# Optimization experiments

Hardware: AMD Instinct MI355X
Metric: run time of the kernel (lower is better)

The kernel has to match this reference:

```python
import jax, jax.numpy as jnp
import numpy as np

B, S, HID = 2, 2048, 2048
H, K, D = 32, 8, 64          # query heads, kv heads, head_dim
G = H // K                   # GQA group size
ROPE_MSCALE = 1.2            # constant rope_mscale applied to q and k
SM_SCALE = 1.0 / (D ** 0.5)  # flash_attn default softmax scale


def rotate_half(x):
    h = x.shape[-1] // 2
    return jnp.concatenate([-x[..., h:], x[..., :h]], axis=-1)


def setup_inputs() -> dict:
    key = jax.random.key(0)
    k1, k2, k3, k4 = jax.random.split(key, 4)
    hidden_states = jax.random.normal(k1, (B, S, HID), dtype=jnp.float32)
    # standard rotary tables: cos/sin of shape [S, D]
    inv_freq = 1.0 / (10000.0 ** (jnp.arange(0, D, 2, dtype=jnp.float32) / D))
    freqs = jnp.outer(jnp.arange(S, dtype=jnp.float32), inv_freq)  # [S, D/2]
    emb = jnp.concatenate([freqs, freqs], axis=-1)                 # [S, D]
    cos, sin = jnp.cos(emb), jnp.sin(emb)
    per_head_scale = 1.0 + 0.1 * jax.random.normal(k2, (B, H), dtype=jnp.float32)
    Wqkv = jax.random.normal(k3, ((H + 2 * K) * D, HID), dtype=jnp.float32) * (HID ** -0.5)
    Wo = jax.random.normal(k4, (HID, H * D), dtype=jnp.float32) * ((H * D) ** -0.5)
    return {"cos": cos, "sin": sin, "hidden_states": hidden_states,
            "per_head_scale": per_head_scale, "Wqkv": Wqkv, "Wo": Wo}


def reference(cos, sin, hidden_states, per_head_scale, Wqkv, Wo):
    # fused QKV projection (CastedLinear, no bias)
    qkv = jnp.einsum('bsh,oh->bso', hidden_states, Wqkv)          # [B,S,(H+2K)*D]
    qkv = qkv.reshape(B, S, H + 2 * K, D)
    q = qkv[:, :, :H]                 # [B,S,H,D]
    k = qkv[:, :, H:H + K]            # [B,S,K,D]
    v = qkv[:, :, H + K:]             # [B,S,K,D]
    # rotary embedding: cos/sin [S,D] -> broadcast over heads via [S,1,D]
    c = cos[:, None, :]
    s_ = sin[:, None, :]
    q = q * c + rotate_half(q) * s_
    k = k * c + rotate_half(k) * s_
    # rope_mscale
    q = q * ROPE_MSCALE
    k = k * ROPE_MSCALE
    # per-head scale on queries: [B,H] -> [B,1,H,1]
    q = q * per_head_scale[:, None, :, None]
    # GQA attention without materializing repeated K/V: group query heads
    qg = q.reshape(B, S, K, G, D)
    scores = jnp.einsum('bqkgd,bskd->bkgqs', qg, k) * SM_SCALE    # [B,K,G,Sq,Sk]
    causal = jnp.arange(S)[:, None] >= jnp.arange(S)[None, :]     # [Sq,Sk]
    scores = jnp.where(causal, scores, jnp.finfo(scores.dtype).min)
    probs = jax.nn.softmax(scores, axis=-1)
    out = jnp.einsum('bkgqs,bskd->bqkgd', probs, v).reshape(B, S, H * D)
    return jnp.einsum('bso,ho->bsh', out, Wo)                     # o_proj
```

## Files before the change

### kernel.cpp

```cpp
#include <hip/hip_runtime.h>
#include <stdint.h>

typedef unsigned short u16;
typedef short short8 __attribute__((ext_vector_type(8)));
typedef float f32x4 __attribute__((ext_vector_type(4)));
typedef uint32_t u32x4 __attribute__((ext_vector_type(4)));

#define S_LEN 2048
#define NQH 32
#define NKH 8
#define DHD 64

__device__ __forceinline__ float b2f(u16 u){
  union { uint32_t i; float f; } c; c.i = ((uint32_t)u) << 16; return c.f;
}
__device__ __forceinline__ u16 f2b(float f){
  union { float f; uint32_t i; } c; c.f = f;
  uint32_t r = c.i + 0x7fffu + ((c.i >> 16) & 1u);
  return (u16)(r >> 16);
}
__device__ __forceinline__ uint32_t cvt_pk_bf16(float lo, float hi){
  uint32_t r;
  asm("v_cvt_pk_bf16_f32 %0, %1, %2" : "=v"(r) : "v"(lo), "v"(hi));
  return r;
}
__device__ __forceinline__ void gload_lds16(const void* g, void* l){
  __builtin_amdgcn_global_load_lds((const __attribute__((address_space(1))) uint32_t*)g,
                                   (__attribute__((address_space(3))) uint32_t*)l, 16, 0, 0);
}

__global__ __launch_bounds__(256) void cvt_all(const float* __restrict__ hs,
                                               const float* __restrict__ wq,
                                               const float* __restrict__ wo,
                                               u16* __restrict__ hsB,
                                               u16* __restrict__ wqB,
                                               u16* __restrict__ woB){
  int i = blockIdx.x * 256 + threadIdx.x;
  const float* src; u16* dst; int off;
  if (i < 2097152)      { src = hs; dst = hsB; off = i; }
  else if (i < 3670016) { src = wq; dst = wqB; off = i - 2097152; }
  else                  { src = wo; dst = woB; off = i - 3670016; }
  float4 v = ((const float4*)src)[off];
  uint2 o;
  o.x = (uint32_t)f2b(v.x) | ((uint32_t)f2b(v.y) << 16);
  o.y = (uint32_t)f2b(v.z) | ((uint32_t)f2b(v.w) << 16);
  ((uint2*)dst)[off] = o;
}

template<int OUT_F32>
__global__ __launch_bounds__(256)
void gemm_bt(const u16* __restrict__ A, const u16* __restrict__ Bm,
             void* __restrict__ Cp, int N, int K)
{
  __shared__ alignas(16) u16 lA[128 * 64];
  __shared__ alignas(16) u16 lB[128 * 64];
  const int tid = threadIdx.x;
  const int w = tid >> 6, l = tid & 63;
  const int lg = l >> 4, lc = l & 15;
  const int wm = w >> 1, wn = w & 1;
  const int m0 = blockIdx.y * 128, n0 = blockIdx.x * 128;
  const int srow = l >> 3, sc = l & 7;
  const size_t ldb = (size_t)K * 2;
  f32x4 acc[4][4] = {};
  const int kiters = K >> 6;
  for (int kt = 0; kt < kiters; ++kt){
    __syncthreads();
#pragma unroll
    for (int i = 0; i < 4; ++i){
      const int row = (i * 4 + w) * 8 + srow;
      const int gc = ((sc ^ (row & 7)) << 4);
      gload_lds16((const char*)A + (size_t)(m0 + row) * ldb + (size_t)kt * 128 + gc,
                  (char*)lA + row * 128 + sc * 16);
    }
#pragma unroll
    for (int i = 0; i < 4; ++i){
      const int row = (i * 4 + w) * 8 + srow;
      const int gc = ((sc ^ (row & 7)) << 4);
      gload_lds16((const char*)Bm + (size_t)(n0 + row) * ldb + (size_t)kt * 128 + gc,
                  (char*)lB + row * 128 + sc * 16);
    }
    __syncthreads();
#pragma unroll
    for (int kk = 0; kk < 2; ++kk){
      short8 af[4], bfr[4];
#pragma unroll
      for (int mi = 0; mi < 4; ++mi){
        const int row = wm * 64 + mi * 16 + lc;
        const int cc = (kk * 4 + lg) ^ (row & 7);
        af[mi] = *(const short8*)((const char*)lA + row * 128 + cc * 16);
      }
#pragma unroll
      for (int ni = 0; ni < 4; ++ni){
        const int row = wn * 64 + ni * 16 + lc;
        const int cc = (kk * 4 + lg) ^ (row & 7);
        bfr[ni] = *(const short8*)((const char*)lB + row * 128 + cc * 16);
      }
#pragma unroll
      for (int mi = 0; mi < 4; ++mi)
#pragma unroll
        for (int ni = 0; ni < 4; ++ni)
          acc[mi][ni] = __builtin_amdgcn_mfma_f32_16x16x32_bf16(af[mi], bfr[ni], acc[mi][ni], 0, 0, 0);
    }
  }
  const int r0 = m0 + wm * 64 + lg * 4;
  const int c0 = n0 + wn * 64 + lc;
#pragma unroll
  for (int mi = 0; mi < 4; ++mi)
#pragma unroll
    for (int ni = 0; ni < 4; ++ni)
#pragma unroll
      for (int j = 0; j < 4; ++j){
        const size_t idx = (size_t)(r0 + mi * 16 + j) * (size_t)N + (size_t)(c0 + ni * 16);
        if (OUT_F32) ((float*)Cp)[idx] = acc[mi][ni][j];
        else         ((u16*)Cp)[idx]  = f2b(acc[mi][ni][j]);
      }
}

__global__ __launch_bounds__(256)
void rope_kernel(const u16* __restrict__ qkv, const float* __restrict__ cosT,
                 const float* __restrict__ sinT, const float* __restrict__ phs,
                 u16* __restrict__ Qo, u16* __restrict__ Ko)
{
  int id = blockIdx.x * 256 + threadIdx.x;
  int b = (id >= 327680) ? 1 : 0;
  int rem = id - b * 327680;
  int head = rem >> 13;
  int s = (rem >> 2) & 2047;
  int d0 = (rem & 3) << 4;
  const u16* src = qkv + (((size_t)(b * S_LEN + s) * 48 + head) << 6);
  uint4 xa = *(const uint4*)(src + d0);
  uint4 xb = *(const uint4*)(src + d0 + 8);
  int d0p = (d0 + 32) & 63;
  uint4 pa = *(const uint4*)(src + d0p);
  uint4 pb = *(const uint4*)(src + d0p + 8);
  const float* cp = cosT + s * 64 + d0;
  const float* sp = sinT + s * 64 + d0;
  const float sgn = (d0 < 32) ? -1.f : 1.f;
  const float kscale = 0.18033688011112042f;
  const float scale = (head < NQH) ? 1.2f * kscale * phs[b * NQH + head] : 1.2f;
  uint32_t xs[4] = {xa.x, xa.y, xa.z, xa.w};
  uint32_t xs2[4] = {xb.x, xb.y, xb.z, xb.w};
  uint32_t ps[4] = {pa.x, pa.y, pa.z, pa.w};
  uint32_t ps2[4] = {pb.x, pb.y, pb.z, pb.w};
  uint32_t ow[8];
#pragma unroll
  for (int k = 0; k < 4; ++k){
    float v0 = b2f((u16)(xs[k] & 0xffff)) * cp[2*k]   + sgn * b2f((u16)(ps[k] & 0xffff)) * sp[2*k];
    float v1 = b2f((u16)(xs[k] >> 16))    * cp[2*k+1] + sgn * b2f((u16)(ps[k] >> 16))    * sp[2*k+1];
    ow[k] = (uint32_t)f2b(v0 * scale) | ((uint32_t)f2b(v1 * scale) << 16);
  }
#pragma unroll
  for (int k = 0; k < 4; ++k){
    float v0 = b2f((u16)(xs2[k] & 0xffff)) * cp[8+2*k]   + sgn * b2f((u16)(ps2[k] & 0xffff)) * sp[8+2*k];
    float v1 = b2f((u16)(xs2[k] >> 16))    * cp[8+2*k+1] + sgn * b2f((u16)(ps2[k] >> 16))    * sp[8+2*k+1];
    ow[4+k] = (uint32_t)f2b(v0 * scale) | ((uint32_t)f2b(v1 * scale) << 16);
  }
  u16* dst;
  if (head < NQH) dst = Qo + (((size_t)(b * NQH + head) * S_LEN + s) << 6) + d0;
  else            dst = Ko + (((size_t)(b * NKH + head - NQH) * S_LEN + s) << 6) + d0;
  uint4 o0 = {ow[0], ow[1], ow[2], ow[3]};
  uint4 o1 = {ow[4], ow[5], ow[6], ow[7]};
  *(uint4*)dst = o0;
  *(uint4*)(dst + 8) = o1;
}

__global__ __launch_bounds__(256)
void vtrans(const u16* __restrict__ qkv, u16* __restrict__ VT)
{
  int bid = blockIdx.x;
  int st = bid & 31, kh = (bid >> 5) & 7, b = bid >> 8;
  __shared__ alignas(16) u16 t[64][72];
  int tid = threadIdx.x;
  int r = tid >> 2, c4 = tid & 3;
  const u16* src = qkv + (((size_t)(b * S_LEN + st * 64 + r) * 48 + 40 + kh) << 6) + c4 * 16;
  *(uint4*)&t[r][c4 * 16]     = *(const uint4*)src;
  *(uint4*)&t[r][c4 * 16 + 8] = *(const uint4*)(src + 8);
  __syncthreads();
  u16 o[16];
#pragma unroll
  for (int i = 0; i < 16; ++i) o[i] = t[c4 * 16 + i][r];
  u16* dst = VT + ((size_t)(b * NKH + kh) * 64 + r) * S_LEN + st * 64 + c4 * 16;
  uint4 o0 = { (uint32_t)o[0] | ((uint32_t)o[1] << 16),  (uint32_t)o[2] | ((uint32_t)o[3] << 16),
               (uint32_t)o[4] | ((uint32_t)o[5] << 16),  (uint32_t)o[6] | ((uint32_t)o[7] << 16) };
  uint4 o1 = { (uint32_t)o[8] | ((uint32_t)o[9] << 16),  (uint32_t)o[10] | ((uint32_t)o[11] << 16),
               (uint32_t)o[12] | ((uint32_t)o[13] << 16),(uint32_t)o[14] | ((uint32_t)o[15] << 16) };
  *(uint4*)dst = o0;
  *(uint4*)(dst + 8) = o1;
}

__global__ __launch_bounds__(256, 2)
void attn_kernel(const u16* __restrict__ Q, const u16* __restrict__ Kr,
                 const u16* __restrict__ VT, u16* __restrict__ Ao)
{
  int bid = blockIdx.x;
  int p  = bid & 15;
  int g  = (bid >> 4) & 3;
  int kh = (bid >> 6) & 7;
  int b  = bid >> 9;
  int h = kh * 4 + g;
  const int qt0 = p, qt1 = 31 - p;

  __shared__ alignas(16) u16 lK[2][128 * 64];
  __shared__ alignas(16) u16 lV[2][64 * 128];

  const int tid = threadIdx.x;
  const int w = tid >> 6, l = tid & 63;
  const int lg = l >> 4, lc = l & 15;

  short8 qf[2][2];
  {
    const u16* qbase = Q + ((size_t)(b * NQH + h) * S_LEN) * 64;
#pragma unroll
    for (int kk = 0; kk < 2; ++kk){
      qf[0][kk] = *(const short8*)(qbase + (size_t)(qt0 * 64 + w * 16 + lc) * 64 + kk * 32 + lg * 8);
      qf[1][kk] = *(const short8*)(qbase + (size_t)(qt1 * 64 + w * 16 + lc) * 64 + kk * 32 + lg * 8);
    }
  }

  const u16* Kb = Kr + (size_t)(b * NKH + kh) * S_LEN * 64;
  const u16* Vb = VT + (size_t)(b * NKH + kh) * 64 * S_LEN;

  f32x4 o[2][4] = {};
  float mrow[2] = {-3.0e38f, -3.0e38f};
  float lsum[2] = {0.f, 0.f};

  const int nt = (qt1 >> 1) + 1;
  const int nt0 = qt0 >> 1;

#define STAGE(T, BSEL) do { \
    _Pragma("unroll") \
    for (int i_ = 0; i_ < 4; ++i_){ \
      const int row_ = i_ * 32 + (tid >> 3); \
      const int ch_  = tid & 7; \
      const int gc_  = ((ch_ ^ (row_ & 7)) << 4); \
      gload_lds16((const char*)(Kb + (size_t)((T) * 128 + row_) * 64) + gc_, \
                  (char*)lK[BSEL] + row_ * 128 + ch_ * 16); \
    } \
    _Pragma("unroll") \
    for (int i_ = 0; i_ < 4; ++i_){ \
      const int row_ = i_ * 16 + (tid >> 4); \
      const int ch_  = tid & 15; \
      const int gc_  = ((ch_ ^ (row_ & 15)) << 4); \
      gload_lds16((const char*)(Vb + (size_t)row_ * S_LEN + (T) * 128) + gc_, \
                  (char*)lV[BSEL] + row_ * 256 + ch_ * 16); \
    } \
  } while (0)

  STAGE(0, 0);

  for (int t = 0; t < nt; ++t){
    const int cur = t & 1;
    const bool act0 = (t <= nt0);
    if (t + 1 < nt){
      STAGE(t + 1, cur ^ 1);
      asm volatile("s_waitcnt vmcnt(8)" ::: "memory");
    } else {
      asm volatile("s_waitcnt vmcnt(0)" ::: "memory");
    }
    __builtin_amdgcn_s_barrier();

    f32x4 sv[2][8] = {};
    __builtin_amdgcn_s_setprio(1);
#pragma unroll
    for (int kk = 0; kk < 2; ++kk){
      short8 kf[8];
#pragma unroll
      for (int nj = 0; nj < 8; ++nj){
        const int row = nj * 16 + lc;
        const int cc = (kk * 4 + lg) ^ (row & 7);
        kf[nj] = *(const short8*)((const char*)lK[cur] + row * 128 + cc * 16);
      }
      if (act0)
#pragma unroll
        for (int nj = 0; nj < 8; ++nj)
          sv[0][nj] = __builtin_amdgcn_mfma_f32_16x16x32_bf16(kf[nj], qf[0][kk], sv[0][nj], 0, 0, 0);
#pragma unroll
      for (int nj = 0; nj < 8; ++nj)
        sv[1][nj] = __builtin_amdgcn_mfma_f32_16x16x32_bf16(kf[nj], qf[1][kk], sv[1][nj], 0, 0, 0);
    }
    __builtin_amdgcn_s_setprio(0);

    uint32_t pw[2][4][4];
#pragma unroll
    for (int c = 0; c < 2; ++c){
      if (c == 0 && !act0) continue;
      const int qt = c ? qt1 : qt0;
      if (t == (qt >> 1)){
        const int qloc = (qt & 1) * 64 + w * 16 + lc;
#pragma unroll
        for (int nj = 0; nj < 8; ++nj)
#pragma unroll
          for (int jj = 0; jj < 4; ++jj){
            const int kloc = nj * 16 + lg * 4 + jj;
            if (kloc > qloc) sv[c][nj][jj] = -3.0e38f;
          }
      }
      float mu = sv[c][0][0];
#pragma unroll
      for (int nj = 0; nj < 8; ++nj)
#pragma unroll
        for (int jj = 0; jj < 4; ++jj) mu = fmaxf(mu, sv[c][nj][jj]);
      mu = fmaxf(mu, __shfl_xor(mu, 16));
      mu = fmaxf(mu, __shfl_xor(mu, 32));
      if (!__all(mu <= mrow[c] + 11.54f)){
        const float mnew = fmaxf(mrow[c], mu);
        const float sf = __builtin_amdgcn_exp2f(mrow[c] - mnew);
        mrow[c] = mnew;
        lsum[c] *= sf;
#pragma unroll
        for (int dn = 0; dn < 4; ++dn)
#pragma unroll
          for (int jj = 0; jj < 4; ++jj) o[c][dn][jj] *= sf;
      }
      const float mcur = mrow[c];
      float ps = 0.f;
#pragma unroll
      for (int nj = 0; nj < 8; ++nj)
#pragma unroll
        for (int jj = 0; jj < 4; ++jj){
          const float pv = __builtin_amdgcn_exp2f(sv[c][nj][jj] - mcur);
          sv[c][nj][jj] = pv;
          ps += pv;
        }
      lsum[c] += ps;
      uint32_t rx[8], ry[8];
#pragma unroll
      for (int nj = 0; nj < 8; ++nj){
        rx[nj] = cvt_pk_bf16(sv[c][nj][0], sv[c][nj][1]);
        ry[nj] = cvt_pk_bf16(sv[c][nj][2], sv[c][nj][3]);
      }
      const int srcA = (lg & 1) * 32 + lc;
      const bool hi = (lg & 2) != 0;
#pragma unroll
      for (int kk2 = 0; kk2 < 4; ++kk2){
        uint32_t x0 = (uint32_t)__shfl((int)rx[kk2 * 2],     srcA);
        uint32_t x1 = (uint32_t)__shfl((int)rx[kk2 * 2 + 1], srcA);
        uint32_t y0 = (uint32_t)__shfl((int)ry[kk2 * 2],     srcA);
        uint32_t y1 = (uint32_t)__shfl((int)ry[kk2 * 2 + 1], srcA);
        pw[c][kk2][0] = hi ? x1 : x0;
        pw[c][kk2][1] = hi ? y1 : y0;
        x0 = (uint32_t)__shfl((int)rx[kk2 * 2],     srcA + 16);
        x1 = (uint32_t)__shfl((int)rx[kk2 * 2 + 1], srcA + 16);
        y0 = (uint32_t)__shfl((int)ry[kk2 * 2],     srcA + 16);
        y1 = (uint32_t)__shfl((int)ry[kk2 * 2 + 1], srcA + 16);
        pw[c][kk2][2] = hi ? x1 : x0;
        pw[c][kk2][3] = hi ? y1 : y0;
      }
    }

    __builtin_amdgcn_s_setprio(1);
#pragma unroll
    for (int kk2 = 0; kk2 < 4; ++kk2){
      short8 vf[4];
#pragma unroll
      for (int dn = 0; dn < 4; ++dn){
        const int row = dn * 16 + lc;
        const int cc = (kk2 * 4 + lg) ^ (row & 15);
        vf[dn] = *(const short8*)((const char*)lV[cur] + row * 256 + cc * 16);
      }
#pragma unroll
      for (int c = 0; c < 2; ++c){
        if (c == 0 && !act0) continue;
        u32x4 pwv = { pw[c][kk2][0], pw[c][kk2][1], pw[c][kk2][2], pw[c][kk2][3] };
        const short8 pb = __builtin_bit_cast(short8, pwv);
#pragma unroll
        for (int dn = 0; dn < 4; ++dn)
          o[c][dn] = __builtin_amdgcn_mfma_f32_16x16x32_bf16(vf[dn], pb, o[c][dn], 0, 0, 0);
      }
    }
    __builtin_amdgcn_s_setprio(0);
    __builtin_amdgcn_s_barrier();
  }
#undef STAGE

#pragma unroll
  for (int c = 0; c < 2; ++c){
    const int qt = c ? qt1 : qt0;
    float ls = lsum[c];
    ls += __shfl_xor(ls, 16);
    ls += __shfl_xor(ls, 32);
    const float inv = 1.f / ls;
    const int sq = qt * 64 + w * 16 + lc;
#pragma unroll
    for (int dn = 0; dn < 4; ++dn){
      uint2 pk;
      pk.x = cvt_pk_bf16(o[c][dn][0] * inv, o[c][dn][1] * inv);
      pk.y = cvt_pk_bf16(o[c][dn][2] * inv, o[c][dn][3] * inv);
      const int col = h * 64 + dn * 16 + lg * 4;
      *(uint2*)&Ao[(size_t)(b * S_LEN + sq) * 2048 + col] = pk;
    }
  }
}

extern "C" void kernel_launch(void* const* d_in, const int* in_sizes, int n_in,
                              void* d_out, int out_size, void* d_ws, size_t ws_size,
                              hipStream_t stream)
{
  const float* cosT = (const float*)d_in[0];
  const float* sinT = (const float*)d_in[1];
  const float* hs   = (const float*)d_in[2];
  const float* phs  = (const float*)d_in[3];
  const float* Wqkv = (const float*)d_in[4];
  const float* Wo   = (const float*)d_in[5];
  float* out = (float*)d_out;
  char* ws = (char*)d_ws;

  u16* hsB   = (u16*)(ws);
  u16* WqkvB = (u16*)(ws + 16777216);
  u16* WoB   = (u16*)(ws + 29360128);
  u16* qkvB  = (u16*)(ws + 37748736);
  u16* Qb    = (u16*)(ws + 62914560);
  u16* Kb    = (u16*)(ws + 79691776);
  u16* VTb   = (u16*)(ws + 83886080);
  u16* Ao    = hsB;

  cvt_all<<<18432, 256, 0, stream>>>(hs, Wqkv, Wo, hsB, WqkvB, WoB);
  gemm_bt<0><<<dim3(24, 32), 256, 0, stream>>>(hsB, WqkvB, (void*)qkvB, 3072, 2048);
  rope_kernel<<<2560, 256, 0, stream>>>(qkvB, cosT, sinT, phs, Qb, Kb);
  vtrans<<<512, 256, 0, stream>>>(qkvB, VTb);
  attn_kernel<<<1024, 256, 0, stream>>>(Qb, Kb, VTb, Ao);
  gemm_bt<1><<<dim3(16, 32), 256, 0, stream>>>(Ao, WoB, (void*)out, 2048, 2048);
}
```

Before: 236.2 us.

## Process two GQA query heads per attention block to reuse staged K/V tiles

Each attention block now handles two query heads that share a KV head, so every K/V tile staged into LDS serves twice as much compute. The grid halves from 1024 to 512 blocks. The softmax/shuffle logic moves into a helper and the mask constant becomes -1e30. The cost is more registers per thread (two sets of accumulators and Q fragments) under launch_bounds(256,2), which risks spills or lower occupancy, plus fewer blocks in flight on the device.

```diff
diff --git a/kernel.cpp b/kernel.cpp
--- a/kernel.cpp
+++ b/kernel.cpp
@@ -10,6 +10,7 @@
 #define NQH 32
 #define NKH 8
 #define DHD 64
+#define MNEG -1.0e30f
 
 __device__ __forceinline__ float b2f(u16 u){
   union { uint32_t i; float f; } c; c.i = ((uint32_t)u) << 16; return c.f;
@@ -188,16 +189,88 @@
   *(uint4*)(dst + 8) = o1;
 }
 
+__device__ __forceinline__ void proc_chunk(f32x4 (&sv)[8], float& mrow, float& lsum,
+                                           f32x4 (&o)[4], uint32_t (&pw)[4][4],
+                                           const int lg, const int lc,
+                                           const bool diag, const int qloc)
+{
+  if (diag){
+#pragma unroll
+    for (int nj = 0; nj < 8; ++nj)
+#pragma unroll
+      for (int jj = 0; jj < 4; ++jj){
+        const int kloc = nj * 16 + lg * 4 + jj;
+        if (kloc > qloc) sv[nj][jj] = MNEG;
+      }
+  }
+  float mu = sv[0][0];
+#pragma unroll
+  for (int nj = 0; nj < 8; ++nj)
+#pragma unroll
+    for (int jj = 0; jj < 4; ++jj) mu = fmaxf(mu, sv[nj][jj]);
+  mu = fmaxf(mu, __shfl_xor(mu, 16));
+  mu = fmaxf(mu, __shfl_xor(mu, 32));
+  if (!__all(mu <= mrow + 11.54f)){
+    const float mnew = fmaxf(mrow, mu);
+    const float sf = __builtin_amdgcn_exp2f(mrow - mnew);
+    mrow = mnew;
+    lsum *= sf;
+#pragma unroll
+    for (int dn = 0; dn < 4; ++dn)
+#pragma unroll
+      for (int jj = 0; jj < 4; ++jj) o[dn][jj] *= sf;
+  }
+  const float mcur = mrow;
+  float ps = 0.f;
+#pragma unroll
+  for (int nj = 0; nj < 8; ++nj)
+#pragma unroll
+    for (int jj = 0; jj < 4; ++jj){
+      const float pv = __builtin_amdgcn_exp2f(sv[nj][jj] - mcur);
+      sv[nj][jj] = pv;
+      ps += pv;
+    }
+  lsum += ps;
+  uint32_t rx[8], ry[8];
+#pragma unroll
+  for (int nj = 0; nj < 8; ++nj){
+    rx[nj] = cvt_pk_bf16(sv[nj][0], sv[nj][1]);
+    ry[nj] = cvt_pk_bf16(sv[nj][2], sv[nj][3]);
+  }
+  const int srcA = (lg & 1) * 32 + lc;
+  const bool hi = (lg & 2) != 0;
+#pragma unroll
+  for (int kk2 = 0; kk2 < 4; ++kk2){
+    uint32_t x0 = (uint32_t)__shfl((int)rx[kk2 * 2],     srcA);
+    uint32_t x1 = (uint32_t)__shfl((int)rx[kk2 * 2 + 1], srcA);
+    uint32_t y0 = (uint32_t)__shfl((int)ry[kk2 * 2],     srcA);
+    uint32_t y1 = (uint32_t)__shfl((int)ry[kk2 * 2 + 1], srcA);
+    pw[kk2][0] = hi ? x1 : x0;
+    pw[kk2][1] = hi ? y1 : y0;
+    x0 = (uint32_t)__shfl((int)rx[kk2 * 2],     srcA + 16);
+    x1 = (uint32_t)__shfl((int)rx[kk2 * 2 + 1], srcA + 16);
+    y0 = (uint32_t)__shfl((int)ry[kk2 * 2],     srcA + 16);
+    y1 = (uint32_t)__shfl((int)ry[kk2 * 2 + 1], srcA + 16);
+    pw[kk2][2] = hi ? x1 : x0;
+    pw[kk2][3] = hi ? y1 : y0;
+  }
+}
+
+__device__ __forceinline__ short8 pw_frag(const uint32_t* pw){
+  u32x4 v = { pw[0], pw[1], pw[2], pw[3] };
+  return __builtin_bit_cast(short8, v);
+}
+
 __global__ __launch_bounds__(256, 2)
 void attn_kernel(const u16* __restrict__ Q, const u16* __restrict__ Kr,
                  const u16* __restrict__ VT, u16* __restrict__ Ao)
 {
   int bid = blockIdx.x;
   int p  = bid & 15;
-  int g  = (bid >> 4) & 3;
-  int kh = (bid >> 6) & 7;
-  int b  = bid >> 9;
-  int h = kh * 4 + g;
+  int gp = (bid >> 4) & 1;
+  int kh = (bid >> 5) & 7;
+  int b  = bid >> 8;
+  int h0 = kh * 4 + gp * 2;
   const int qt0 = p, qt1 = 31 - p;
 
   __shared__ alignas(16) u16 lK[2][128 * 64];
@@ -207,22 +280,25 @@
   const int w = tid >> 6, l = tid & 63;
   const int lg = l >> 4, lc = l & 15;
 
-  short8 qf[2][2];
+  short8 qf[2][2][2];
   {
-    const u16* qbase = Q + ((size_t)(b * NQH + h) * S_LEN) * 64;
-#pragma unroll
-    for (int kk = 0; kk < 2; ++kk){
-      qf[0][kk] = *(const short8*)(qbase + (size_t)(qt0 * 64 + w * 16 + lc) * 64 + kk * 32 + lg * 8);
-      qf[1][kk] = *(const short8*)(qbase + (size_t)(qt1 * 64 + w * 16 + lc) * 64 + kk * 32 + lg * 8);
+#pragma unroll
+    for (int hh = 0; hh < 2; ++hh){
+      const u16* qbase = Q + ((size_t)(b * NQH + h0 + hh) * S_LEN) * 64;
+#pragma unroll
+      for (int kk = 0; kk < 2; ++kk){
+        qf[hh][0][kk] = *(const short8*)(qbase + (size_t)(qt0 * 64 + w * 16 + lc) * 64 + kk * 32 + lg * 8);
+        qf[hh][1][kk] = *(const short8*)(qbase + (size_t)(qt1 * 64 + w * 16 + lc) * 64 + kk * 32 + lg * 8);
+      }
     }
   }
 
   const u16* Kb = Kr + (size_t)(b * NKH + kh) * S_LEN * 64;
   const u16* Vb = VT + (size_t)(b * NKH + kh) * 64 * S_LEN;
 
-  f32x4 o[2][4] = {};
-  float mrow[2] = {-3.0e38f, -3.0e38f};
-  float lsum[2] = {0.f, 0.f};
+  f32x4 o[2][2][4] = {};
+  float mrow[2][2] = {{MNEG, MNEG}, {MNEG, MNEG}};
+  float lsum[2][2] = {{0.f, 0.f}, {0.f, 0.f}};
 
   const int nt = (qt1 >> 1) + 1;
   const int nt0 = qt0 >> 1;
@@ -259,137 +335,82 @@
     }
     __builtin_amdgcn_s_barrier();
 
-    f32x4 sv[2][8] = {};
-    __builtin_amdgcn_s_setprio(1);
-#pragma unroll
-    for (int kk = 0; kk < 2; ++kk){
-      short8 kf[8];
-#pragma unroll
-      for (int nj = 0; nj < 8; ++nj){
-        const int row = nj * 16 + lc;
-        const int cc = (kk * 4 + lg) ^ (row & 7);
-        kf[nj] = *(const short8*)((const char*)lK[cur] + row * 128 + cc * 16);
-      }
+#pragma unroll
+    for (int hh = 0; hh < 2; ++hh){
+      f32x4 sv[2][8] = {};
+      __builtin_amdgcn_s_setprio(1);
+#pragma unroll
+      for (int kk = 0; kk < 2; ++kk){
+        short8 kf[8];
+#pragma unroll
+        for (int nj = 0; nj < 8; ++nj){
+          const int row = nj * 16 + lc;
+          const int cc = (kk * 4 + lg) ^ (row & 7);
+          kf[nj] = *(const short8*)((const char*)lK[cur] + row * 128 + cc * 16);
+        }
+        if (act0)
+#pragma unroll
+          for (int nj = 0; nj < 8; ++nj)
+            sv[0][nj] = __builtin_amdgcn_mfma_f32_16x16x32_bf16(kf[nj], qf[hh][0][kk], sv[0][nj], 0, 0, 0);
+#pragma unroll
+        for (int nj = 0; nj < 8; ++nj)
+          sv[1][nj] = __builtin_amdgcn_mfma_f32_16x16x32_bf16(kf[nj], qf[hh][1][kk], sv[1][nj], 0, 0, 0);
+      }
+      __builtin_amdgcn_s_setprio(0);
+
+      uint32_t pw[2][4][4];
       if (act0)
-#pragma unroll
-        for (int nj = 0; nj < 8; ++nj)
-          sv[0][nj] = __builtin_amdgcn_mfma_f32_16x16x32_bf16(kf[nj], qf[0][kk], sv[0][nj], 0, 0, 0);
-#pragma unroll
-      for (int nj = 0; nj < 8; ++nj)
-        sv[1][nj] = __builtin_amdgcn_mfma_f32_16x16x32_bf16(kf[nj], qf[1][kk], sv[1][nj], 0, 0, 0);
-    }
-    __builtin_amdgcn_s_setprio(0);
-
-    uint32_t pw[2][4][4];
+        proc_chunk(sv[0], mrow[hh][0], lsum[hh][0], o[hh][0], pw[0], lg, lc,
+                   t == (qt0 >> 1), (qt0 & 1) * 64 + w * 16 + lc);
+      proc_chunk(sv[1], mrow[hh][1], lsum[hh][1], o[hh][1], pw[1], lg, lc,
+                 t == (qt1 >> 1), (qt1 & 1) * 64 + w * 16 + lc);
+
+      __builtin_amdgcn_s_setprio(1);
+#pragma unroll
+      for (int kk2 = 0; kk2 < 4; ++kk2){
+        short8 vf[4];
+#pragma unroll
+        for (int dn = 0; dn < 4; ++dn){
+          const int row = dn * 16 + lc;
+          const int cc = (kk2 * 4 + lg) ^ (row & 15);
+          vf[dn] = *(const short8*)((const char*)lV[cur] + row * 256 + cc * 16);
+        }
+        if (act0){
+          const short8 pb0 = pw_frag(pw[0][kk2]);
+#pragma unroll
+          for (int dn = 0; dn < 4; ++dn)
+            o[hh][0][dn] = __builtin_amdgcn_mfma_f32_16x16x32_bf16(vf[dn], pb0, o[hh][0][dn], 0, 0, 0);
+        }
+        const short8 pb1 = pw_frag(pw[1][kk2]);
+#pragma unroll
+        for (int dn = 0; dn < 4; ++dn)
+          o[hh][1][dn] = __builtin_amdgcn_mfma_f32_16x16x32_bf16(vf[dn], pb1, o[hh][1][dn], 0, 0, 0);
+      }
+      __builtin_amdgcn_s_setprio(0);
+    }
+    __builtin_amdgcn_s_barrier();
+  }
+#undef STAGE
+
+#pragma unroll
+  for (int hh = 0; hh < 2; ++hh)
 #pragma unroll
     for (int c = 0; c < 2; ++c){
-      if (c == 0 && !act0) continue;
       const int qt = c ? qt1 : qt0;
-      if (t == (qt >> 1)){
-        const int qloc = (qt & 1) * 64 + w * 16 + lc;
-#pragma unroll
-        for (int nj = 0; nj < 8; ++nj)
-#pragma unroll
-          for (int jj = 0; jj < 4; ++jj){
-            const int kloc = nj * 16 + lg * 4 + jj;
-            if (kloc > qloc) sv[c][nj][jj] = -3.0e38f;
-          }
-      }
-      float mu = sv[c][0][0];
-#pragma unroll
-      for (int nj = 0; nj < 8; ++nj)
-#pragma unroll
-        for (int jj = 0; jj < 4; ++jj) mu = fmaxf(mu, sv[c][nj][jj]);
-      mu = fmaxf(mu, __shfl_xor(mu, 16));
-      mu = fmaxf(mu, __shfl_xor(mu, 32));
-      if (!__all(mu <= mrow[c] + 11.54f)){
-        const float mnew = fmaxf(mrow[c], mu);
-        const float sf = __builtin_amdgcn_exp2f(mrow[c] - mnew);
-        mrow[c] = mnew;
-        lsum[c] *= sf;
-#pragma unroll
-        for (int dn = 0; dn < 4; ++dn)
-#pragma unroll
-          for (int jj = 0; jj < 4; ++jj) o[c][dn][jj] *= sf;
-      }
-      const float mcur = mrow[c];
-      float ps = 0.f;
-#pragma unroll
-      for (int nj = 0; nj < 8; ++nj)
-#pragma unroll
-        for (int jj = 0; jj < 4; ++jj){
-          const float pv = __builtin_amdgcn_exp2f(sv[c][nj][jj] - mcur);
-          sv[c][nj][jj] = pv;
-          ps += pv;
-        }
-      lsum[c] += ps;
-      uint32_t rx[8], ry[8];
-#pragma unroll
-      for (int nj = 0; nj < 8; ++nj){
-        rx[nj] = cvt_pk_bf16(sv[c][nj][0], sv[c][nj][1]);
-        ry[nj] = cvt_pk_bf16(sv[c][nj][2], sv[c][nj][3]);
-      }
-      const int srcA = (lg & 1) * 32 + lc;
-      const bool hi = (lg & 2) != 0;
-#pragma unroll
-      for (int kk2 = 0; kk2 < 4; ++kk2){
-        uint32_t x0 = (uint32_t)__shfl((int)rx[kk2 * 2],     srcA);
-        uint32_t x1 = (uint32_t)__shfl((int)rx[kk2 * 2 + 1], srcA);
-        uint32_t y0 = (uint32_t)__shfl((int)ry[kk2 * 2],     srcA);
-        uint32_t y1 = (uint32_t)__shfl((int)ry[kk2 * 2 + 1], srcA);
-        pw[c][kk2][0] = hi ? x1 : x0;
-        pw[c][kk2][1] = hi ? y1 : y0;
-        x0 = (uint32_t)__shfl((int)rx[kk2 * 2],     srcA + 16);
-        x1 = (uint32_t)__shfl((int)rx[kk2 * 2 + 1], srcA + 16);
-        y0 = (uint32_t)__shfl((int)ry[kk2 * 2],     srcA + 16);
-        y1 = (uint32_t)__shfl((int)ry[kk2 * 2 + 1], srcA + 16);
-        pw[c][kk2][2] = hi ? x1 : x0;
-        pw[c][kk2][3] = hi ? y1 : y0;
-      }
-    }
-
-    __builtin_amdgcn_s_setprio(1);
-#pragma unroll
-    for (int kk2 = 0; kk2 < 4; ++kk2){
-      short8 vf[4];
+      float ls = lsum[hh][c];
+      ls += __shfl_xor(ls, 16);
+      ls += __shfl_xor(ls, 32);
+      const float inv = 1.f / ls;
+      const int sq = qt * 64 + w * 16 + lc;
 #pragma unroll
       for (int dn = 0; dn < 4; ++dn){
-        const int row = dn * 16 + lc;
-        const int cc = (kk2 * 4 + lg) ^ (row & 15);
-        vf[dn] = *(const short8*)((const char*)lV[cur] + row * 256 + cc * 16);
-      }
-#pragma unroll
-      for (int c = 0; c < 2; ++c){
-        if (c == 0 && !act0) continue;
-        u32x4 pwv = { pw[c][kk2][0], pw[c][kk2][1], pw[c][kk2][2], pw[c][kk2][3] };
-        const short8 pb = __builtin_bit_cast(short8, pwv);
-#pragma unroll
-        for (int dn = 0; dn < 4; ++dn)
-          o[c][dn] = __builtin_amdgcn_mfma_f32_16x16x32_bf16(vf[dn], pb, o[c][dn], 0, 0, 0);
-      }
-    }
-    __builtin_amdgcn_s_setprio(0);
-    __builtin_amdgcn_s_barrier();
-  }
-#undef STAGE
-
-#pragma unroll
-  for (int c = 0; c < 2; ++c){
-    const int qt = c ? qt1 : qt0;
-    float ls = lsum[c];
-    ls += __shfl_xor(ls, 16);
-    ls += __shfl_xor(ls, 32);
-    const float inv = 1.f / ls;
-    const int sq = qt * 64 + w * 16 + lc;
-#pragma unroll
-    for (int dn = 0; dn < 4; ++dn){
-      uint2 pk;
-      pk.x = cvt_pk_bf16(o[c][dn][0] * inv, o[c][dn][1] * inv);
-      pk.y = cvt_pk_bf16(o[c][dn][2] * inv, o[c][dn][3] * inv);
-      const int col = h * 64 + dn * 16 + lg * 4;
-      *(uint2*)&Ao[(size_t)(b * S_LEN + sq) * 2048 + col] = pk;
-    }
-  }
+        uint2 pk;
+        pk.x = cvt_pk_bf16(o[hh][c][dn][0] * inv, o[hh][c][dn][1] * inv);
+        pk.y = cvt_pk_bf16(o[hh][c][dn][2] * inv, o[hh][c][dn][3] * inv);
+        const int col = (h0 + hh) * 64 + dn * 16 + lg * 4;
+        *(uint2*)&Ao[(size_t)(b * S_LEN + sq) * 2048 + col] = pk;
+      }
+    }
 }
 
 extern "C" void kernel_launch(void* const* d_in, const int* in_sizes, int n_in,
@@ -418,6 +439,6 @@
   gemm_bt<0><<<dim3(24, 32), 256, 0, stream>>>(hsB, WqkvB, (void*)qkvB, 3072, 2048);
   rope_kernel<<<2560, 256, 0, stream>>>(qkvB, cosT, sinT, phs, Qb, Kb);
   vtrans<<<512, 256, 0, stream>>>(qkvB, VTb);
-  attn_kernel<<<1024, 256, 0, stream>>>(Qb, Kb, VTb, Ao);
+  attn_kernel<<<512, 256, 0, stream>>>(Qb, Kb, VTb, Ao);
   gemm_bt<1><<<dim3(16, 32), 256, 0, stream>>>(Ao, WoB, (void*)out, 2048, 2048);
 }
```

New measurement: 361.3 us. 53.0% more time.
